# Kernel tuning notes

Measured on AMD Instinct MI355X. Metric: run time of the kernel, lower is better.

The kernel has to match this reference:

```python
import jax, jax.numpy as jnp
import numpy as np

# ---------- spherical offset pattern (setup-time, numpy, exact port) ----------

def _get_xy(dp, dt):
    t, c = np.tan, np.cos
    return np.array([
        [(-t(dt), 1/c(dt)*t(dp)), (0, t(dp)), (t(dt), 1/c(dt)*t(dp))],
        [(-t(dt), 0),             (1, 1),     (t(dt), 0)],
        [(-t(dt), -1/c(dt)*t(dp)), (0, -t(dp)), (t(dt), -1/c(dt)*t(dp))]])


def _cal_offset(h, w, r, c):
    phi = -((r + 0.5) / h * np.pi - np.pi / 2)
    theta = (c + 0.5) / w * 2 * np.pi - np.pi
    xys = _get_xy(np.pi / h, 2 * np.pi / w)
    x, y = xys[..., 0], xys[..., 1]
    rho = np.sqrt(x ** 2 + y ** 2)
    v = np.arctan(rho)
    new_phi = np.arcsin(np.cos(v) * np.sin(phi) + y * np.sin(v) * np.cos(phi) / rho)
    new_theta = theta + np.arctan(x * np.sin(v) / (rho * np.cos(phi) * np.cos(v) - y * np.sin(phi) * np.sin(v)))
    new_r = (-new_phi + np.pi / 2) * h / np.pi - 0.5
    new_c = (new_theta + np.pi) * w / 2 / np.pi - 0.5
    new_c = (new_c + w) % w
    res = np.stack([new_r, new_c], axis=-1)
    res[1, 1] = (r, c)
    for i in range(3):
        for j in range(3):
            res[i, j, 0] -= (r + i - 1)
            res[i, j, 1] -= (c + j - 1)
    return res.reshape(-1)  # (18,) ordered k=i*3+j, pairs (dy, dx)


def _offsets_map(h, w):
    with np.errstate(all='ignore'):
        co = np.array([[_cal_offset(h, w, i, j) for j in range(w)] for i in range(h)])
    return co.transpose(2, 0, 1)  # (18, h, w)


# ---------- jax forward ----------

def _bilinear_gather(x, py, px):
    # x: [B,C,H,W]; py/px: [K,H,W] float sample coords. Zero padding outside.
    B, C, H, W = x.shape
    y0 = jnp.floor(py); x0 = jnp.floor(px)
    wy = py - y0; wx = px - x0
    y0i = y0.astype(jnp.int32); x0i = x0.astype(jnp.int32)
    xf = x.reshape(B, C, H * W)

    def corner(yi, xi, wgt):
        valid = (yi >= 0) & (yi < H) & (xi >= 0) & (xi < W)
        idx = (jnp.clip(yi, 0, H - 1) * W + jnp.clip(xi, 0, W - 1)).reshape(-1)
        v = jnp.take(xf, idx, axis=2).reshape(B, C, *py.shape)  # [B,C,K,H,W]
        return v * (wgt * valid.astype(x.dtype))[None, None]

    return (corner(y0i,     x0i,     (1 - wy) * (1 - wx)) +
            corner(y0i,     x0i + 1, (1 - wy) * wx) +
            corner(y0i + 1, x0i,     wy * (1 - wx)) +
            corner(y0i + 1, x0i + 1, wy * wx))


def _forward(x, weight, bias, w_down, w_up, scale, offset):
    B, C, H, W = x.shape
    O = weight.shape[0]
    # frozen dense 3x3 conv (stride 1, pad 1)
    h = jax.lax.conv_general_dilated(
        x, weight, window_strides=(1, 1), padding=((1, 1), (1, 1)),
        dimension_numbers=('NCHW', 'OIHW', 'NCHW'))
    h = h + bias[None, :, None, None]
    # deform_conv2d with fixed spherical offsets (offset: [18,H,W] -> [9,2,H,W])
    off = offset.reshape(9, 2, H, W)
    dy, dx_ = off[:, 0], off[:, 1]
    kk = jnp.arange(9)
    ki = (kk // 3).astype(x.dtype); kj = (kk % 3).astype(x.dtype)
    pp = jnp.arange(H, dtype=x.dtype); qq = jnp.arange(W, dtype=x.dtype)
    py = pp[None, :, None] - 1.0 + ki[:, None, None] + dy  # [9,H,W]
    px = qq[None, None, :] - 1.0 + kj[:, None, None] + dx_
    sampled = _bilinear_gather(x, py, px)                   # [B,C,9,H,W]
    dconv = jnp.einsum('bckhw,ock->bohw', sampled, weight.reshape(O, C, 9))
    dconv = dconv + bias[None, :, None, None]
    # concat + dual 1x1 conv LoRA fusion + scaled residual
    cat = jnp.concatenate([dconv, h], axis=1)               # [B,2O,H,W]
    down = jnp.einsum('bchw,oc->bohw', cat, w_down)
    up = jnp.einsum('bchw,oc->bohw', down, w_up)
    return h + scale * up


def setup_inputs() -> dict:
    key = jax.random.key(0)
    ks = jax.random.split(key, 6)
    B, C, O, H, W = 4, 320, 320, 64, 64
    low = max(O // 1, 1)
    x = jax.random.normal(ks[0], (B, C, H, W), dtype=jnp.float32)
    weight = jax.random.normal(ks[1], (O, C, 3, 3), dtype=jnp.float32) * 0.02
    bias = jax.random.normal(ks[2], (O,), dtype=jnp.float32) * 0.02
    w_down = jax.random.normal(ks[3], (low, 2 * O), dtype=jnp.float32) * 0.02
    w_up = jax.random.normal(ks[4], (O, low), dtype=jnp.float32) * 0.02
    scale = jnp.asarray(1.0, dtype=jnp.float32)
    offset = jnp.asarray(_offsets_map(H, W), dtype=jnp.float32)  # [18,H,W]
    return {'x': x, 'weight': weight, 'bias': bias, 'w_down': w_down,
            'w_up': w_up, 'scale': scale, 'offset': offset}


def reference(x, weight, bias, w_down, w_up, scale, offset):
    return _forward(x, weight, bias, w_down, w_up, scale, offset)
```

## Files before the change

### kernel.cpp

```cpp
#include <hip/hip_runtime.h>
#include <stdint.h>


typedef __attribute__((ext_vector_type(4))) float f32x4;
typedef __attribute__((ext_vector_type(8))) short bf16x8;

typedef __attribute__((address_space(1))) const unsigned int uint_as1;
typedef __attribute__((address_space(3))) unsigned int uint_as3;

__device__ __forceinline__ void gl_lds16(const void* g, void* l) {
    __builtin_amdgcn_global_load_lds((uint_as1*)g, (uint_as3*)l, 16, 0, 0);
}

__device__ __forceinline__ unsigned short f2b(float f) {
    union { float f; uint32_t u; } v; v.f = f;
    uint32_t r = (v.u + 0x7FFFu + ((v.u >> 16) & 1u)) >> 16;
    return (unsigned short)r;
}
__device__ __forceinline__ float b2f(unsigned short h) {
    union { uint32_t u; float f; } v; v.u = ((uint32_t)h) << 16;
    return v.f;
}
__device__ __forceinline__ float b2f_lo(uint32_t u) {
    union { uint32_t u; float f; } v; v.u = u << 16;
    return v.f;
}
__device__ __forceinline__ float b2f_hi(uint32_t u) {
    union { uint32_t u; float f; } v; v.u = u & 0xFFFF0000u;
    return v.f;
}
__device__ __forceinline__ uint32_t pack2(float lo, float hi) {
    return (uint32_t)f2b(lo) | ((uint32_t)f2b(hi) << 16);
}

#define TAP8(AC, tv, wvx) \
    AC[0] += wvx * b2f_lo((uint32_t)tv.x); AC[1] += wvx * b2f_hi((uint32_t)tv.x); \
    AC[2] += wvx * b2f_lo((uint32_t)tv.y); AC[3] += wvx * b2f_hi((uint32_t)tv.y); \
    AC[4] += wvx * b2f_lo((uint32_t)tv.z); AC[5] += wvx * b2f_hi((uint32_t)tv.z); \
    AC[6] += wvx * b2f_lo((uint32_t)tv.w); AC[7] += wvx * b2f_hi((uint32_t)tv.w);

__global__ __launch_bounds__(256) void k_prep(const float* __restrict__ off,
                                              const float* __restrict__ w,
                                              const float* __restrict__ wd,
                                              const float* __restrict__ wu,
                                              const float* __restrict__ x,
                                              uint32_t* __restrict__ oIdx,
                                              float* __restrict__ oW,
                                              unsigned short* __restrict__ Wr2,
                                              unsigned short* __restrict__ W2,
                                              unsigned short* __restrict__ Xb)
{
    const int bx = blockIdx.x, tid = threadIdx.x;
    if (bx < 144) {
        int gid = bx * 256 + tid;
        int k = gid >> 12;
        int p = gid & 4095;
        int i = p >> 6, j = p & 63;
        float dy = off[(2 * k) * 4096 + p];
        float dx = off[(2 * k + 1) * 4096 + p];
        float py = (float)(i - 1 + k / 3) + dy;
        float px = (float)(j - 1 + k % 3) + dx;
        float fy = floorf(py), fx = floorf(px);
        float wy = py - fy, wx = px - fx;
        fy = fminf(fmaxf(fy, -100.f), 100.f);
        fx = fminf(fmaxf(fx, -100.f), 100.f);
        int y0 = (int)fy, x0 = (int)fx;
        float vy0 = (y0 >= 0 && y0 < 64) ? 1.f : 0.f;
        float vy1 = (y0 >= -1 && y0 < 63) ? 1.f : 0.f;
        float vx0 = (x0 >= 0 && x0 < 64) ? 1.f : 0.f;
        float vx1 = (x0 >= -1 && x0 < 63) ? 1.f : 0.f;
        float w00 = (1.f - wy) * (1.f - wx) * vy0 * vx0;
        float w01 = (1.f - wy) * wx * vy0 * vx1;
        float w10 = wy * (1.f - wx) * vy1 * vx0;
        float w11 = wy * wx * vy1 * vx1;
        int ya = min(max(y0, 0), 63), yb = min(max(y0 + 1, 0), 63);
        int xa = min(max(x0, 0), 63), xb = min(max(x0 + 1, 0), 63);
        oIdx[gid * 2 + 0] = (uint32_t)(ya * 64 + xa) | ((uint32_t)(ya * 64 + xb) << 16);
        oIdx[gid * 2 + 1] = (uint32_t)(yb * 64 + xa) | ((uint32_t)(yb * 64 + xb) << 16);
        oW[gid * 4 + 0] = w00;
        oW[gid * 4 + 1] = w01;
        oW[gid * 4 + 2] = w10;
        oW[gid * 4 + 3] = w11;
    } else if (bx < 594) {
        int gid = (bx - 144) * 256 + tid;
        int cb = gid / 2880, m = gid - cb * 2880;
        int k = m / 320, o = m - k * 320;
        float v[8];
        #pragma unroll
        for (int cl = 0; cl < 8; ++cl) {
            int c = cb * 8 + cl;
            v[cl] = w[((size_t)o * 320 + c) * 9 + k];
        }
        int4 st;
        st.x = (int)pack2(v[0], v[1]);
        st.y = (int)pack2(v[2], v[3]);
        st.z = (int)pack2(v[4], v[5]);
        st.w = (int)pack2(v[6], v[7]);
        *(int4*)(Wr2 + (size_t)gid * 8) = st;
    } else if (bx < 1554) {
        int gid = (bx - 594) * 256 + tid;
        int o = gid / 640, kk2 = gid % 640;
        float a0 = 0.f, a1 = 0.f, a2 = 0.f, a3 = 0.f;
        if (o < 320) {
            const float* wuo = wu + (size_t)o * 320;
            for (int l = 0; l < 320; l += 4) {
                float4 u4 = *(const float4*)(wuo + l);
                a0 += u4.x * wd[(size_t)(l + 0) * 640 + kk2];
                a1 += u4.y * wd[(size_t)(l + 1) * 640 + kk2];
                a2 += u4.z * wd[(size_t)(l + 2) * 640 + kk2];
                a3 += u4.w * wd[(size_t)(l + 3) * 640 + kk2];
            }
        }
        W2[(size_t)((kk2 >> 3) * 384 + o) * 8 + (kk2 & 7)] = f2b((a0 + a1) + (a2 + a3));
    } else {
        int bz = bx - 1554;
        int sp = bz & 3, rest = bz >> 2;
        int gl = rest % 40, b = rest / 40;
        const float* xb = x + ((size_t)b * 320 + gl * 8) * 4096;
        unsigned short* xpb = Xb + ((size_t)gl * 16384 + b * 4096) * 8;
        #pragma unroll
        for (int i = 0; i < 4; ++i) {
            int px = sp * 1024 + i * 256 + tid;
            float v0 = xb[0 * 4096 + px], v1 = xb[1 * 4096 + px];
            float v2 = xb[2 * 4096 + px], v3 = xb[3 * 4096 + px];
            float v4 = xb[4 * 4096 + px], v5 = xb[5 * 4096 + px];
            float v6 = xb[6 * 4096 + px], v7 = xb[7 * 4096 + px];
            int4 st;
            st.x = (int)pack2(v0, v1);
            st.y = (int)pack2(v2, v3);
            st.z = (int)pack2(v4, v5);
            st.w = (int)pack2(v6, v7);
            *(int4*)(xpb + (size_t)px * 8) = st;
        }
    }
}

__global__ __launch_bounds__(256, 3) void k_zgemm(const unsigned short* __restrict__ Xb,
                                                  const unsigned short* __restrict__ Wr2,
                                                  unsigned short* __restrict__ Z)
{
    __shared__ __align__(16) unsigned short Bs[2][8 * 128 * 8];
    const int tid = threadIdx.x;
    const int n0 = blockIdx.x * 128, m0 = blockIdx.y * 160;
    const int lane = tid & 63, w = tid >> 6;
    const int wm = w & 1, wn = w >> 1;
    const int quad = lane >> 4, nl = lane & 15;
    const unsigned short* Abase = Wr2 + ((size_t)quad * 2880 + m0 + wm * 80 + nl) * 8;

#define STAGE_B(buf, s1) do { \
    _Pragma("unroll") \
    for (int q_ = 0; q_ < 4; ++q_) { \
        int u_ = tid + q_ * 256; \
        int row_ = u_ >> 7, nn_ = n0 + (u_ & 127); \
        gl_lds16(Xb + ((size_t)((s1) * 8 + row_) * 16384 + nn_) * 8, &Bs[buf][u_ * 8]); \
    } \
} while (0)

    f32x4 acc[5][4];
    #pragma unroll
    for (int mt = 0; mt < 5; ++mt)
        #pragma unroll
        for (int nt = 0; nt < 4; ++nt)
            acc[mt][nt] = 0.f;

    STAGE_B(0, 0);
    asm volatile("s_waitcnt vmcnt(0)" ::: "memory");
    __builtin_amdgcn_s_barrier();
    __builtin_amdgcn_sched_barrier(0);

    for (int s = 0; s < 5; ++s) {
        const int p = s & 1, np = p ^ 1;
        bf16x8 a[2][5];
        #pragma unroll
        for (int kc = 0; kc < 2; ++kc)
            #pragma unroll
            for (int mt = 0; mt < 5; ++mt)
                a[kc][mt] = *(const bf16x8*)(Abase
                    + ((size_t)((s * 8 + kc * 4) * 2880) + mt * 16) * 8);
        if (s < 4) STAGE_B(np, s + 1);
        __builtin_amdgcn_sched_barrier(0);
        #pragma unroll
        for (int kc = 0; kc < 2; ++kc) {
            bf16x8 bf[4];
            #pragma unroll
            for (int nt = 0; nt < 4; ++nt)
                bf[nt] = *(const bf16x8*)&Bs[p][((kc * 4 + quad) * 128 + wn * 64 + nt * 16 + nl) * 8];
            #pragma unroll
            for (int mt = 0; mt < 5; ++mt)
                #pragma unroll
                for (int nt = 0; nt < 4; ++nt)
                    acc[mt][nt] = __builtin_amdgcn_mfma_f32_16x16x32_bf16(a[kc][mt], bf[nt], acc[mt][nt], 0, 0, 0);
        }
        asm volatile("s_waitcnt vmcnt(0)" ::: "memory");
        __builtin_amdgcn_s_barrier();
        __builtin_amdgcn_sched_barrier(0);
    }

    #pragma unroll
    for (int mt = 0; mt < 5; ++mt) {
        int o0m = m0 + wm * 80 + mt * 16 + quad * 4;
        #pragma unroll
        for (int nt = 0; nt < 4; ++nt) {
            int n2 = n0 + wn * 64 + nt * 16 + nl;
            unsigned short* pp = Z + ((size_t)(o0m >> 3) * 16384 + n2) * 8 + (o0m & 7);
            ushort4 st;
            st.x = f2b(acc[mt][nt][0]);
            st.y = f2b(acc[mt][nt][1]);
            st.z = f2b(acc[mt][nt][2]);
            st.w = f2b(acc[mt][nt][3]);
            *(ushort4*)pp = st;
        }
    }
#undef STAGE_B
}

__global__ __launch_bounds__(512) void k_blend(const unsigned short* __restrict__ Z,
                                               const uint32_t* __restrict__ oIdx,
                                               const float* __restrict__ oW,
                                               const float* __restrict__ bias,
                                               unsigned short* __restrict__ Cc)
{
    __shared__ __align__(16) unsigned short Zp[4096 * 8];
    const int tid = threadIdx.x;
    const int sp = blockIdx.x, og = blockIdx.y, b = blockIdx.z;
    const int px0 = sp * 1024;

    float ac[2][8], ah[2][8];
    {
        float4 b0 = *(const float4*)&bias[og * 8];
        float4 b1 = *(const float4*)&bias[og * 8 + 4];
        #pragma unroll
        for (int j = 0; j < 2; ++j) {
            ac[j][0] = b0.x; ac[j][1] = b0.y; ac[j][2] = b0.z; ac[j][3] = b0.w;
            ac[j][4] = b1.x; ac[j][5] = b1.y; ac[j][6] = b1.z; ac[j][7] = b1.w;
            #pragma unroll
            for (int q = 0; q < 8; ++q) ah[j][q] = ac[j][q];
        }
    }

    for (int k = 0; k < 9; ++k) {
        const unsigned short* Zplane = Z + ((size_t)(k * 40 + og) * 16384 + b * 4096) * 8;
        #pragma unroll
        for (int q = 0; q < 8; ++q) {
            int u = tid + q * 512;
            gl_lds16(Zplane + (size_t)u * 8, &Zp[u * 8]);
        }
        asm volatile("s_waitcnt vmcnt(0)" ::: "memory");
        __builtin_amdgcn_s_barrier();

        #pragma unroll
        for (int j = 0; j < 2; ++j) {
            int lpx = j * 512 + tid;
            int px = px0 + lpx;
            int gi = (k << 12) + px;
            uint32_t i0 = oIdx[gi * 2];
            uint32_t i1 = oIdx[gi * 2 + 1];
            float4 wv = *(const float4*)&oW[(size_t)gi * 4];
            int r = px >> 6, c0 = px & 63;
            int rr = r + k / 3 - 1, cc = c0 + k % 3 - 1;
            bool valid = (rr >= 0) & (rr < 64) & (cc >= 0) & (cc < 64);
            int hidx = valid ? (rr * 64 + cc) : 0;
            float hw = valid ? 1.f : 0.f;
            int4 t0 = *(const int4*)&Zp[(size_t)(i0 & 0xFFFFu) * 8];
            int4 t1 = *(const int4*)&Zp[(size_t)(i0 >> 16) * 8];
            int4 t2 = *(const int4*)&Zp[(size_t)(i1 & 0xFFFFu) * 8];
            int4 t3 = *(const int4*)&Zp[(size_t)(i1 >> 16) * 8];
            int4 th = *(const int4*)&Zp[(size_t)hidx * 8];
            TAP8(ac[j], t0, wv.x) TAP8(ac[j], t1, wv.y)
            TAP8(ac[j], t2, wv.z) TAP8(ac[j], t3, wv.w)
            TAP8(ah[j], th, hw)
        }
        __builtin_amdgcn_s_barrier();
    }

    #pragma unroll
    for (int j = 0; j < 2; ++j) {
        int px = px0 + j * 512 + tid;
        int4 sd, sh;
        sd.x = (int)pack2(ac[j][0], ac[j][1]); sd.y = (int)pack2(ac[j][2], ac[j][3]);
        sd.z = (int)pack2(ac[j][4], ac[j][5]); sd.w = (int)pack2(ac[j][6], ac[j][7]);
        sh.x = (int)pack2(ah[j][0], ah[j][1]); sh.y = (int)pack2(ah[j][2], ah[j][3]);
        sh.z = (int)pack2(ah[j][4], ah[j][5]); sh.w = (int)pack2(ah[j][6], ah[j][7]);
        unsigned short* cp = Cc + ((size_t)og * 32768 + b * 4096 + px) * 8;
        *(int4*)cp = sd;
        *(int4*)(cp + 16384 * 8) = sh;
    }
}

__global__ __launch_bounds__(256) void k_final(const unsigned short* __restrict__ W2,
                                               const unsigned short* __restrict__ Cc,
                                               const float* __restrict__ scale,
                                               float* __restrict__ out)
{
    __shared__ __align__(16) unsigned short As[2][8 * 160 * 8];
    __shared__ __align__(16) unsigned short Bs[2][8 * 64 * 8];
    const int tid = threadIdx.x;
    const int n0 = blockIdx.x * 64, m0 = blockIdx.y * 160;
    const int lane = tid & 63, w = tid >> 6;
    const int wm = w & 1, wn = w >> 1;
    const int quad = lane >> 4, nl = lane & 15;

#define STAGEF(buf, s1) do { \
    _Pragma("unroll") \
    for (int q_ = 0; q_ < 5; ++q_) { \
        int u_ = tid + q_ * 256; \
        int kq_ = u_ / 160, m_ = u_ - kq_ * 160; \
        gl_lds16(W2 + ((size_t)(((s1) * 8 + kq_) * 384 + m0 + m_)) * 8, &As[buf][u_ * 8]); \
    } \
    { \
        int h_off_ = ((s1) < 5) ? 0 : 16384; \
        int gq_ = ((s1) < 5) ? (s1) * 8 : ((s1) - 5) * 8; \
        _Pragma("unroll") \
        for (int q_ = 0; q_ < 2; ++q_) { \
            int u_ = tid + q_ * 256; \
            int row_ = u_ >> 6, nn_ = n0 + (u_ & 63); \
            gl_lds16(Cc + ((size_t)(gq_ + row_) * 32768 + h_off_ + nn_) * 8, &Bs[buf][u_ * 8]); \
        } \
    } \
} while (0)

    f32x4 acc[5][2];
    #pragma unroll
    for (int mt = 0; mt < 5; ++mt)
        #pragma unroll
        for (int nt = 0; nt < 2; ++nt)
            acc[mt][nt] = 0.f;

    STAGEF(0, 0);
    asm volatile("s_waitcnt vmcnt(0)" ::: "memory");
    __builtin_amdgcn_s_barrier();
    __builtin_amdgcn_sched_barrier(0);

    for (int s = 0; s < 10; ++s) {
        const int p = s & 1, np = p ^ 1;
        if (s < 9) STAGEF(np, s + 1);
        __builtin_amdgcn_sched_barrier(0);
        #pragma unroll
        for (int kc = 0; kc < 2; ++kc) {
            bf16x8 a[5], bf[2];
            #pragma unroll
            for (int mt = 0; mt < 5; ++mt)
                a[mt] = *(const bf16x8*)&As[p][((kc * 4 + quad) * 160 + wm * 80 + mt * 16 + nl) * 8];
            #pragma unroll
            for (int nt = 0; nt < 2; ++nt)
                bf[nt] = *(const bf16x8*)&Bs[p][((kc * 4 + quad) * 64 + wn * 32 + nt * 16 + nl) * 8];
            #pragma unroll
            for (int mt = 0; mt < 5; ++mt)
                #pragma unroll
                for (int nt = 0; nt < 2; ++nt)
                    acc[mt][nt] = __builtin_amdgcn_mfma_f32_16x16x32_bf16(a[mt], bf[nt], acc[mt][nt], 0, 0, 0);
        }
        asm volatile("s_waitcnt vmcnt(0)" ::: "memory");
        __builtin_amdgcn_s_barrier();
        __builtin_amdgcn_sched_barrier(0);
    }

    float sc = scale[0];
    #pragma unroll
    for (int mt = 0; mt < 5; ++mt) {
        int o0 = m0 + wm * 80 + mt * 16 + quad * 4;
        #pragma unroll
        for (int nt = 0; nt < 2; ++nt) {
            int n = n0 + wn * 32 + nt * 16 + nl;
            int b = n >> 12, px = n & 4095;
            ushort4 hv = *(const ushort4*)(Cc + ((size_t)(o0 >> 3) * 32768 + n + 16384) * 8 + (o0 & 7));
            size_t base = ((size_t)(b * 320 + o0)) * 4096 + px;
            out[base]            = b2f(hv.x) + sc * acc[mt][nt][0];
            out[base + 4096]     = b2f(hv.y) + sc * acc[mt][nt][1];
            out[base + 2 * 4096] = b2f(hv.z) + sc * acc[mt][nt][2];
            out[base + 3 * 4096] = b2f(hv.w) + sc * acc[mt][nt][3];
        }
    }
#undef STAGEF
}

extern "C" void kernel_launch(void* const* d_in, const int* in_sizes, int n_in,
                              void* d_out, int out_size, void* d_ws, size_t ws_size,
                              hipStream_t stream)
{
    const float* x      = (const float*)d_in[0];
    const float* weight = (const float*)d_in[1];
    const float* bias   = (const float*)d_in[2];
    const float* w_down = (const float*)d_in[3];
    const float* w_up   = (const float*)d_in[4];
    const float* scale  = (const float*)d_in[5];
    const float* offset = (const float*)d_in[6];
    char* ws = (char*)d_ws;
    unsigned short* Cc    = (unsigned short*)(ws + 0);
    unsigned short* Wr2   = (unsigned short*)(ws + 25165824);
    unsigned short* W2    = (unsigned short*)(ws + 27377664);
    uint32_t*       oI    = (uint32_t*)(ws + 27869184);
    float*          oWt   = (float*)(ws + 28164096);
    unsigned short* Xb    = (unsigned short*)(ws + 28758016);
    unsigned short* Z     = (unsigned short*)(ws + 39909376);
    float* out = (float*)d_out;

    hipLaunchKernelGGL(k_prep, dim3(2194), dim3(256), 0, stream,
                       offset, weight, w_down, w_up, x, oI, oWt, Wr2, W2, Xb);
    hipLaunchKernelGGL(k_zgemm, dim3(128, 18), dim3(256), 0, stream,
                       Xb, Wr2, Z);
    hipLaunchKernelGGL(k_blend, dim3(4, 40, 4), dim3(512), 0, stream,
                       Z, oI, oWt, bias, Cc);
    hipLaunchKernelGGL(k_final, dim3(256, 2), dim3(256), 0, stream,
                       W2, Cc, scale, out);
}
```

Measured before the change: 216.1 us.

## Double-buffer Z plane staging in blend kernel and remove redundant per-block reloads

The blend kernel now uses one 1024-thread block per (output group, batch) covering all 4096 pixels, instead of four blocks that each reloaded the same Z plane. It double-buffers the per-tap Z plane in LDS so the async load of tap k+1 overlaps the gather and FMA work of tap k. This cuts redundant global loads fourfold but shrinks the grid from 640 to 160 blocks, which could underfill the GPU's CUs. It also doubles LDS per block to 128KB and adds register pressure from 4 pixels per thread.

```diff
diff --git a/kernel.cpp b/kernel.cpp
--- a/kernel.cpp
+++ b/kernel.cpp
@@ -214,23 +214,31 @@
 #undef STAGE_B
 }
 
-__global__ __launch_bounds__(512) void k_blend(const unsigned short* __restrict__ Z,
-                                               const uint32_t* __restrict__ oIdx,
-                                               const float* __restrict__ oW,
-                                               const float* __restrict__ bias,
-                                               unsigned short* __restrict__ Cc)
+__global__ __launch_bounds__(1024) void k_blend(const unsigned short* __restrict__ Z,
+                                                const uint32_t* __restrict__ oIdx,
+                                                const float* __restrict__ oW,
+                                                const float* __restrict__ bias,
+                                                unsigned short* __restrict__ Cc)
 {
-    __shared__ __align__(16) unsigned short Zp[4096 * 8];
+    __shared__ __align__(16) unsigned short Zp[2][4096 * 8];
     const int tid = threadIdx.x;
-    const int sp = blockIdx.x, og = blockIdx.y, b = blockIdx.z;
-    const int px0 = sp * 1024;
-
-    float ac[2][8], ah[2][8];
+    const int og = blockIdx.x, b = blockIdx.y;
+
+#define STAGE_Z(buf, k1) do { \
+    const unsigned short* Zplane_ = Z + ((size_t)((k1) * 40 + og) * 16384 + b * 4096) * 8; \
+    _Pragma("unroll") \
+    for (int q_ = 0; q_ < 4; ++q_) { \
+        int u_ = tid + q_ * 1024; \
+        gl_lds16(Zplane_ + (size_t)u_ * 8, &Zp[buf][u_ * 8]); \
+    } \
+} while (0)
+
+    float ac[4][8], ah[4][8];
     {
         float4 b0 = *(const float4*)&bias[og * 8];
         float4 b1 = *(const float4*)&bias[og * 8 + 4];
         #pragma unroll
-        for (int j = 0; j < 2; ++j) {
+        for (int j = 0; j < 4; ++j) {
             ac[j][0] = b0.x; ac[j][1] = b0.y; ac[j][2] = b0.z; ac[j][3] = b0.w;
             ac[j][4] = b1.x; ac[j][5] = b1.y; ac[j][6] = b1.z; ac[j][7] = b1.w;
             #pragma unroll
@@ -238,20 +246,17 @@
         }
     }
 
+    STAGE_Z(0, 0);
+    asm volatile("s_waitcnt vmcnt(0)" ::: "memory");
+    __builtin_amdgcn_s_barrier();
+
     for (int k = 0; k < 9; ++k) {
-        const unsigned short* Zplane = Z + ((size_t)(k * 40 + og) * 16384 + b * 4096) * 8;
-        #pragma unroll
-        for (int q = 0; q < 8; ++q) {
-            int u = tid + q * 512;
-            gl_lds16(Zplane + (size_t)u * 8, &Zp[u * 8]);
-        }
-        asm volatile("s_waitcnt vmcnt(0)" ::: "memory");
-        __builtin_amdgcn_s_barrier();
-
-        #pragma unroll
-        for (int j = 0; j < 2; ++j) {
-            int lpx = j * 512 + tid;
-            int px = px0 + lpx;
+        const int p = k & 1, np = p ^ 1;
+        if (k < 8) STAGE_Z(np, k + 1);
+
+        #pragma unroll
+        for (int j = 0; j < 4; ++j) {
+            int px = j * 1024 + tid;
             int gi = (k << 12) + px;
             uint32_t i0 = oIdx[gi * 2];
             uint32_t i1 = oIdx[gi * 2 + 1];
@@ -261,21 +266,22 @@
             bool valid = (rr >= 0) & (rr < 64) & (cc >= 0) & (cc < 64);
             int hidx = valid ? (rr * 64 + cc) : 0;
             float hw = valid ? 1.f : 0.f;
-            int4 t0 = *(const int4*)&Zp[(size_t)(i0 & 0xFFFFu) * 8];
-            int4 t1 = *(const int4*)&Zp[(size_t)(i0 >> 16) * 8];
-            int4 t2 = *(const int4*)&Zp[(size_t)(i1 & 0xFFFFu) * 8];
-            int4 t3 = *(const int4*)&Zp[(size_t)(i1 >> 16) * 8];
-            int4 th = *(const int4*)&Zp[(size_t)hidx * 8];
+            int4 t0 = *(const int4*)&Zp[p][(size_t)(i0 & 0xFFFFu) * 8];
+            int4 t1 = *(const int4*)&Zp[p][(size_t)(i0 >> 16) * 8];
+            int4 t2 = *(const int4*)&Zp[p][(size_t)(i1 & 0xFFFFu) * 8];
+            int4 t3 = *(const int4*)&Zp[p][(size_t)(i1 >> 16) * 8];
+            int4 th = *(const int4*)&Zp[p][(size_t)hidx * 8];
             TAP8(ac[j], t0, wv.x) TAP8(ac[j], t1, wv.y)
             TAP8(ac[j], t2, wv.z) TAP8(ac[j], t3, wv.w)
             TAP8(ah[j], th, hw)
         }
+        asm volatile("s_waitcnt vmcnt(0)" ::: "memory");
         __builtin_amdgcn_s_barrier();
     }
 
     #pragma unroll
-    for (int j = 0; j < 2; ++j) {
-        int px = px0 + j * 512 + tid;
+    for (int j = 0; j < 4; ++j) {
+        int px = j * 1024 + tid;
         int4 sd, sh;
         sd.x = (int)pack2(ac[j][0], ac[j][1]); sd.y = (int)pack2(ac[j][2], ac[j][3]);
         sd.z = (int)pack2(ac[j][4], ac[j][5]); sd.w = (int)pack2(ac[j][6], ac[j][7]);
@@ -285,6 +291,7 @@
         *(int4*)cp = sd;
         *(int4*)(cp + 16384 * 8) = sh;
     }
+#undef STAGE_Z
 }
 
 __global__ __launch_bounds__(256) void k_final(const unsigned short* __restrict__ W2,
@@ -399,7 +406,7 @@
                        offset, weight, w_down, w_up, x, oI, oWt, Wr2, W2, Xb);
     hipLaunchKernelGGL(k_zgemm, dim3(128, 18), dim3(256), 0, stream,
                        Xb, Wr2, Z);
-    hipLaunchKernelGGL(k_blend, dim3(4, 40, 4), dim3(512), 0, stream,
+    hipLaunchKernelGGL(k_blend, dim3(40, 4), dim3(1024), 0, stream,
                        Z, oI, oWt, bias, Cc);
     hipLaunchKernelGGL(k_final, dim3(256, 2), dim3(256), 0, stream,
                        W2, Cc, scale, out);
```

Result: faster. 204.7 us (-5.3%).
